# Optimization experiments

Measured on AMD Instinct MI355X. Metric: run time of the kernel, lower is better.

## Reference

```python
import jax, jax.numpy as jnp
import numpy as np

EMBED_DIM = 1024
NUM_HEADS = 16
HEAD_DIM = EMBED_DIM // NUM_HEADS


def setup_inputs() -> dict:
    key = jax.random.key(0)
    ks = jax.random.split(key, 9)
    D = EMBED_DIM
    s = 1.0 / np.sqrt(D)
    x = jax.random.normal(ks[0], (2, 2048, D), dtype=jnp.float32)
    Wq = jax.random.uniform(ks[1], (D, D), jnp.float32, -s, s)
    bq = jax.random.uniform(ks[2], (D,), jnp.float32, -s, s)
    Wk = jax.random.uniform(ks[3], (D, D), jnp.float32, -s, s)
    bk = jax.random.uniform(ks[4], (D,), jnp.float32, -s, s)
    Wv = jax.random.uniform(ks[5], (D, D), jnp.float32, -s, s)
    bv = jax.random.uniform(ks[6], (D,), jnp.float32, -s, s)
    Wo = jax.random.uniform(ks[7], (D, D), jnp.float32, -s, s)
    bo = jax.random.uniform(ks[8], (D,), jnp.float32, -s, s)
    return {"x": x, "Wq": Wq, "bq": bq, "Wk": Wk, "bk": bk,
            "Wv": Wv, "bv": bv, "Wo": Wo, "bo": bo}


def reference(x, Wq, bq, Wk, bk, Wv, bv, Wo, bo):
    B, N, D = x.shape
    H, Dh = NUM_HEADS, HEAD_DIM
    # QKV projections (weights stored as [in, out] = torch W.T)
    q = (x @ Wq + bq).reshape(B, N, H, Dh).transpose(0, 2, 1, 3)  # b h n d
    k = (x @ Wk + bk).reshape(B, N, H, Dh).transpose(0, 2, 1, 3)
    v = (x @ Wv + bv).reshape(B, N, H, Dh).transpose(0, 2, 1, 3)
    # NOTE: original divides by head_dim (not sqrt(head_dim))
    scores = jnp.einsum('bhnd,bhmd->bhnm', q, k) / Dh
    probs = jax.nn.softmax(scores, axis=-1)
    out = jnp.einsum('bhnm,bhmd->bhnd', probs, v)  # b h n d
    out = out.transpose(0, 2, 1, 3).reshape(B, N, D)
    return out @ Wo + bo
```

## Files before the change

### kernel.cpp

```cpp
#include <hip/hip_runtime.h>
#include <hip/hip_bf16.h>

constexpr int EMBED = 1024;
constexpr int NHEAD = 16;
constexpr int HDIM  = 64;
constexpr int BATCH = 2;
constexpr int SEQ   = 2048;
constexpr int MROWS = BATCH * SEQ;
constexpr int NKB   = EMBED / 32;
constexpr int NT    = SEQ / 64;

typedef __attribute__((ext_vector_type(8)))  short          bf8;
typedef __attribute__((ext_vector_type(8)))  unsigned short us8;
typedef __attribute__((ext_vector_type(16))) float          f32x16;
typedef __attribute__((ext_vector_type(2)))  int            i32x2;

__device__ __forceinline__ unsigned short f2bf(float f) {
  unsigned u = __float_as_uint(f);
  u += 0x7fffu + ((u >> 16) & 1u);
  return (unsigned short)(u >> 16);
}
__device__ __forceinline__ float bf2f(unsigned short h) {
  return __uint_as_float((unsigned)h << 16);
}
__device__ __forceinline__ void async16(const void* g, void* l) {
  __builtin_amdgcn_global_load_lds(
      (const __attribute__((address_space(1))) unsigned int*)g,
      (__attribute__((address_space(3))) unsigned int*)l, 16, 0, 0);
}
__device__ __forceinline__ i32x2 swap32(int a, int b) {
  return __builtin_amdgcn_permlane32_swap(a, b, false, false);
}
__device__ __forceinline__ unsigned cvt2(float a, float b) {
  union { __hip_bfloat162 bb; unsigned u; } cv;
  cv.bb = __float22bfloat162_rn(float2{a, b});
  return cv.u;
}
__device__ __forceinline__ void bar_pre() {
  __builtin_amdgcn_s_barrier();
  __builtin_amdgcn_sched_barrier(0);
}
__device__ __forceinline__ void bar_post() {
  __builtin_amdgcn_sched_barrier(0);
  __builtin_amdgcn_s_barrier();
}

__global__ __launch_bounds__(256) void pack_x_k(
    const float* __restrict__ x, char* __restrict__ Xp)
{
  int sid = blockIdx.x * 256 + threadIdx.x;
  int s = sid & 7, t = (sid >> 3) & 31, u = sid >> 8;
  int c = s ^ (u & 7);
  int par = c >> 2, kq = c & 3;
  const float* src = x + (size_t)(2 * u + par) * EMBED + t * 32 + kq * 8;
  us8 o;
  #pragma unroll
  for (int e = 0; e < 8; ++e) o[e] = f2bf(src[e]);
  *(us8*)(Xp + ((size_t)sid << 4)) = o;
}

__global__ __launch_bounds__(256) void pack_w_lds_k(
    const float* __restrict__ W0, const float* __restrict__ W1,
    const float* __restrict__ W2, const float* __restrict__ W3,
    char* __restrict__ Wpk)
{
  __shared__ float LDSf[8 * 1032];
  const int blk = blockIdx.x;
  const int tid = threadIdx.x;
  const int y = blk >> 7, r = blk & 127, t = r >> 2, q = r & 3;
  const float* W = (y == 0) ? W0 : (y == 1) ? W1 : (y == 2) ? W2 : W3;
  char* op = Wpk + ((size_t)y << 21);

  #pragma unroll
  for (int it = 0; it < 8; ++it) {
    int f4 = it * 256 + tid;
    int row = f4 >> 8, col4 = (f4 & 255) << 2;
    float4 v = *(const float4*)(W + (size_t)(t * 32 + q * 8 + row) * EMBED + col4);
    *(float4*)(&LDSf[row * 1032 + col4]) = v;
  }
  __syncthreads();

  #pragma unroll
  for (int it = 0; it < 4; ++it) {
    int sid2 = it * 256 + tid;
    int u = sid2 >> 1, par = sid2 & 1;
    int s = ((par << 2) | q) ^ (u & 7);
    us8 o;
    #pragma unroll
    for (int e = 0; e < 8; ++e) o[e] = f2bf(LDSf[e * 1032 + 2 * u + par]);
    *(us8*)(op + (((size_t)(u << 8) + (t << 3) + s) << 4)) = o;
  }
}

__global__ __launch_bounds__(256) void gemm_qkv_fused_k(
    const char* __restrict__ Apk, const char* __restrict__ Wpk,
    const float* __restrict__ B0, const float* __restrict__ B1, const float* __restrict__ B2,
    unsigned short* __restrict__ Qbf, unsigned short* __restrict__ Kbf,
    unsigned short* __restrict__ Vt)
{
  __shared__ __align__(16) char lds[65536];

  const int tid  = threadIdx.x;
  const int lane = tid & 63;
  const int wid  = tid >> 6;
  const int wr   = wid >> 1, wc = wid & 1;
  const int ln31 = lane & 31, lhalf = lane >> 5;

  const int bid = blockIdx.x;
  const int swz = (bid & 7) * 32 + (bid >> 3);
  const int rp  = swz >> 3, cb = swz & 7;

  const int M0 = rp * 128, N0 = cb * 128;
  const int U0 = M0 >> 1, V0 = N0 >> 1;

  const char* ab[2]; const char* wbase[2]; int ldoff[2];
  #pragma unroll
  for (int i = 0; i < 2; ++i) {
    int idx = i * 256 + tid;
    int ul = idx >> 3, sl = idx & 7;
    ab[i]    = Apk + ((size_t)(U0 + ul) << 12) + (sl << 4);
    wbase[i] = Wpk + ((size_t)(V0 + ul) << 12) + (sl << 4);
    ldoff[i] = i * 4096 + (tid >> 6) * 1024;
  }

  f32x16 acc[3][2][2];
  #pragma unroll
  for (int z = 0; z < 3; ++z)
    #pragma unroll
    for (int mi = 0; mi < 2; ++mi)
      #pragma unroll
      for (int ni = 0; ni < 2; ++ni)
        #pragma unroll
        for (int q = 0; q < 16; ++q) acc[z][mi][ni][q] = 0.f;

  #pragma unroll
  for (int i = 0; i < 2; ++i) {
    async16(ab[i], lds + ldoff[i]);
    #pragma unroll
    for (int z = 0; z < 3; ++z)
      async16(wbase[i] + ((size_t)z << 21), lds + 8192 + z * 8192 + ldoff[i]);
  }

  for (int t = 0; t < NKB; ++t) {
    const int c = t & 1;
    if (t + 1 < NKB) {
      const int off = (t + 1) << 7;
      #pragma unroll
      for (int i = 0; i < 2; ++i) {
        async16(ab[i] + off, lds + (c ^ 1) * 32768 + ldoff[i]);
        #pragma unroll
        for (int z = 0; z < 3; ++z)
          async16(wbase[i] + ((size_t)z << 21) + off,
                  lds + (c ^ 1) * 32768 + 8192 + z * 8192 + ldoff[i]);
      }
      asm volatile("s_waitcnt vmcnt(8)" ::: "memory");
    } else {
      asm volatile("s_waitcnt vmcnt(0)" ::: "memory");
    }
    bar_pre();
    const char* Ab = lds + c * 32768;
    const char* Wb = Ab + 8192;
    #pragma unroll
    for (int kb = 0; kb < 2; ++kb) {
      const int kq = (kb << 1) | lhalf;
      bf8 a[2];
      #pragma unroll
      for (int mi = 0; mi < 2; ++mi) {
        int m = wr * 64 + mi * 32 + ln31;
        int u = m >> 1;
        int s = (((m & 1) << 2) | kq) ^ (u & 7);
        a[mi] = *(const bf8*)(Ab + u * 128 + s * 16);
      }
      #pragma unroll
      for (int z = 0; z < 3; ++z) {
        bf8 b[2];
        #pragma unroll
        for (int ni = 0; ni < 2; ++ni) {
          int n = wc * 64 + ni * 32 + ln31;
          int u = n >> 1;
          int s = (((n & 1) << 2) | kq) ^ (u & 7);
          b[ni] = *(const bf8*)(Wb + z * 8192 + u * 128 + s * 16);
        }
        #pragma unroll
        for (int mi = 0; mi < 2; ++mi)
          #pragma unroll
          for (int ni = 0; ni < 2; ++ni)
            acc[z][mi][ni] = __builtin_amdgcn_mfma_f32_32x32x16_bf16(
                a[mi], b[ni], acc[z][mi][ni], 0, 0, 0);
      }
    }
    bar_post();
  }

  #pragma unroll
  for (int z = 0; z < 2; ++z) {
    unsigned short* Cb = (z == 0) ? Qbf : Kbf;
    const float* Bv = (z == 0) ? B0 : B1;
    const float sc = (z == 0) ? (1.44269504088896f / 64.0f) : 1.0f;
    #pragma unroll
    for (int ni = 0; ni < 2; ++ni) {
      int col = N0 + wc * 64 + ni * 32 + ln31;
      float bb = Bv[col];
      #pragma unroll
      for (int mi = 0; mi < 2; ++mi)
        #pragma unroll
        for (int r = 0; r < 16; ++r) {
          int row = M0 + wr * 64 + mi * 32 + (r & 3) + ((r >> 2) << 3) + (lhalf << 2);
          Cb[(size_t)row * EMBED + col] = f2bf((acc[z][mi][ni][r] + bb) * sc);
        }
    }
  }
  {
    const int tg0 = (M0 & 2047) >> 6;
    const int bb  = M0 >> 11;
    #pragma unroll
    for (int ni = 0; ni < 2; ++ni) {
      int col = N0 + wc * 64 + ni * 32 + ln31;
      int hh = col >> 6, dl = col & 63;
      float bv = B2[col];
      size_t base2 = (((size_t)(bb * 16 + hh)) << 17) + ((size_t)(tg0 + wr) << 12) + (dl << 6);
      unsigned pkq[2][4][2];
      #pragma unroll
      for (int mi = 0; mi < 2; ++mi)
        #pragma unroll
        for (int rg = 0; rg < 4; ++rg) {
          pkq[mi][rg][0] = cvt2(acc[2][mi][ni][4 * rg + 0] + bv, acc[2][mi][ni][4 * rg + 1] + bv);
          pkq[mi][rg][1] = cvt2(acc[2][mi][ni][4 * rg + 2] + bv, acc[2][mi][ni][4 * rg + 3] + bv);
        }
      #pragma unroll
      for (int gk = 0; gk < 8; ++gk) {
        const int mi = gk >> 2, rg = gk & 3;
        i32x2 e0 = swap32((int)pkq[mi][rg][0], (int)pkq[mi][rg][0]);
        i32x2 e1 = swap32((int)pkq[mi][rg][1], (int)pkq[mi][rg][1]);
        int g = gk ^ (dl & 7);
        if ((g >> 2) == lhalf) {
          union { unsigned u[4]; us8 v; } o;
          o.u[0] = (unsigned)e0[0]; o.u[1] = (unsigned)e1[0];
          o.u[2] = (unsigned)e0[1]; o.u[3] = (unsigned)e1[1];
          *(us8*)(Vt + base2 + (g << 3)) = o.v;
        }
      }
    }
  }
}

__global__ __launch_bounds__(256) void gemm_out_bf16_k(
    const char* __restrict__ Apk, const char* __restrict__ Wpk,
    const float* __restrict__ Bv, float* __restrict__ Cf)
{
  __shared__ __align__(16) char lds[65536];

  const int tid  = threadIdx.x;
  const int lane = tid & 63;
  const int wid  = tid >> 6;
  const int wr   = wid >> 1, wc = wid & 1;
  const int ln31 = lane & 31, lhalf = lane >> 5;

  const int bid = blockIdx.x;
  const int swz = (bid & 7) * 32 + (bid >> 3);
  const int rp  = swz >> 3, cb = swz & 7;

  const int M0 = rp * 128, N0 = cb * 128;
  const int U0 = M0 >> 1, V0 = N0 >> 1;

  const char* ab[4]; const char* wb[4]; int ldoff[4];
  #pragma unroll
  for (int i = 0; i < 4; ++i) {
    int idx = i * 256 + tid;
    int ul = idx >> 4, tt = (idx >> 3) & 1, sl = idx & 7;
    ab[i] = Apk + ((size_t)(U0 + ul) << 12) + (tt << 7) + (sl << 4);
    wb[i] = Wpk + ((size_t)(V0 + ul) << 12) + (tt << 7) + (sl << 4);
    ldoff[i] = i * 4096 + (tid >> 6) * 1024;
  }

  f32x16 acc[2][2];
  #pragma unroll
  for (int mi = 0; mi < 2; ++mi)
    #pragma unroll
    for (int ni = 0; ni < 2; ++ni)
      #pragma unroll
      for (int q = 0; q < 16; ++q) acc[mi][ni][q] = 0.f;

  #pragma unroll
  for (int i = 0; i < 4; ++i) {
    async16(ab[i], lds + ldoff[i]);
    async16(wb[i], lds + 16384 + ldoff[i]);
  }

  for (int T = 0; T < NKB / 2; ++T) {
    const int c = T & 1;
    if (T + 1 < NKB / 2) {
      const int off = (T + 1) << 8;
      #pragma unroll
      for (int i = 0; i < 4; ++i) {
        async16(ab[i] + off, lds + (c ^ 1) * 32768 + ldoff[i]);
        async16(wb[i] + off, lds + (c ^ 1) * 32768 + 16384 + ldoff[i]);
      }
      asm volatile("s_waitcnt vmcnt(8)" ::: "memory");
    } else {
      asm volatile("s_waitcnt vmcnt(0)" ::: "memory");
    }
    bar_pre();
    const char* Ab = lds + c * 32768;
    const char* Wb = Ab + 16384;
    #pragma unroll
    for (int tt = 0; tt < 2; ++tt) {
      #pragma unroll
      for (int kb = 0; kb < 2; ++kb) {
        const int kq = (kb << 1) | lhalf;
        bf8 a[2], b[2];
        #pragma unroll
        for (int mi = 0; mi < 2; ++mi) {
          int m = wr * 64 + mi * 32 + ln31;
          int ul = m >> 1;
          int s = (((m & 1) << 2) | kq) ^ (ul & 7);
          a[mi] = *(const bf8*)(Ab + ul * 256 + tt * 128 + s * 16);
        }
        #pragma unroll
        for (int ni = 0; ni < 2; ++ni) {
          int n = wc * 64 + ni * 32 + ln31;
          int ul = n >> 1;
          int s = (((n & 1) << 2) | kq) ^ (ul & 7);
          b[ni] = *(const bf8*)(Wb + ul * 256 + tt * 128 + s * 16);
        }
        #pragma unroll
        for (int mi = 0; mi < 2; ++mi)
          #pragma unroll
          for (int ni = 0; ni < 2; ++ni)
            acc[mi][ni] = __builtin_amdgcn_mfma_f32_32x32x16_bf16(
                a[mi], b[ni], acc[mi][ni], 0, 0, 0);
      }
    }
    bar_post();
  }

  #pragma unroll
  for (int ni = 0; ni < 2; ++ni) {
    int col = N0 + wc * 64 + ni * 32 + ln31;
    float bb = Bv[col];
    #pragma unroll
    for (int mi = 0; mi < 2; ++mi)
      #pragma unroll
      for (int r = 0; r < 16; ++r) {
        int row = M0 + wr * 64 + mi * 32 + (r & 3) + ((r >> 2) << 3) + (lhalf << 2);
        Cf[(size_t)row * EMBED + col] = acc[mi][ni][r] + bb;
      }
  }
}

__global__ __launch_bounds__(512) void attn_mfma_k(
    const unsigned short* __restrict__ Qb, const unsigned short* __restrict__ Kb,
    const char* __restrict__ Vt, char* __restrict__ A2)
{
  __shared__ __align__(16) char lds[65536];

  const int bid = blockIdx.x;
  const int swz = (bid & 7) * 64 + (bid >> 3);
  const int qt = swz & 15, h = (swz >> 4) & 15, b = swz >> 8;

  const int tid  = threadIdx.x;
  const int kw   = tid >> 8;
  const int tidg = tid & 255;
  const int lane = tid & 63;
  const int qw   = (tid >> 6) & 3;
  const int ln31 = lane & 31, lh = lane >> 5;
  const int l7   = ln31 & 7;

  const int q0 = qt * 128;
  const int sbase = kw * 32768;
  const int T0 = kw * 16;

  bf8 qf[4];
  {
    const size_t qoff = (size_t)(b * SEQ + q0 + qw * 32 + ln31) * EMBED + h * HDIM;
    #pragma unroll
    for (int kd = 0; kd < 4; ++kd)
      qf[kd] = *(const bf8*)(Qb + qoff + (2 * kd + lh) * 8);
  }

  const unsigned short* ksrc[2];
  const char* vtb = Vt + ((size_t)(b * 16 + h) << 18);
  int ldoff[2];
  #pragma unroll
  for (int i = 0; i < 2; ++i) {
    int idx = i * 256 + tidg;
    int r = idx >> 3, s7 = idx & 7;
    int un = s7 ^ (r & 7);
    ksrc[i] = Kb + (size_t)(b * SEQ + r) * EMBED + h * HDIM + un * 8;
    ldoff[i] = i * 4096 + (tidg >> 6) * 1024;
  }

  #pragma unroll
  for (int i = 0; i < 2; ++i) {
    async16(ksrc[i] + (size_t)(T0 * 64) * EMBED, lds + sbase + ldoff[i]);
    async16(vtb + (T0 << 13) + ((i * 256 + tidg) << 4), lds + sbase + 8192 + ldoff[i]);
  }

  const bf8 ones = {0x3F80, 0x3F80, 0x3F80, 0x3F80, 0x3F80, 0x3F80, 0x3F80, 0x3F80};
  f32x16 z16;
  #pragma unroll
  for (int r = 0; r < 16; ++r) z16[r] = 0.f;

  f32x16 oacc[2], oacc3;
  #pragma unroll
  for (int df = 0; df < 2; ++df)
    #pragma unroll
    for (int r = 0; r < 16; ++r) oacc[df][r] = 0.f;
  oacc3 = z16;

  for (int it = 0; it < NT / 2; ++it) {
    const int c = it & 1;
    if (it + 1 < NT / 2) {
      const int tn = T0 + it + 1;
      #pragma unroll
      for (int i = 0; i < 2; ++i) {
        async16(ksrc[i] + (size_t)(tn * 64) * EMBED, lds + sbase + (c ^ 1) * 16384 + ldoff[i]);
        async16(vtb + (tn << 13) + ((i * 256 + tidg) << 4),
                lds + sbase + (c ^ 1) * 16384 + 8192 + ldoff[i]);
      }
      asm volatile("s_waitcnt vmcnt(4)" ::: "memory");
    } else {
      asm volatile("s_waitcnt vmcnt(0)" ::: "memory");
    }
    bar_pre();
    const char* Kbuf = lds + sbase + c * 16384;
    const char* Vbuf = Kbuf + 8192;

    f32x16 sacc[2];
    __builtin_amdgcn_s_setprio(1);
    #pragma unroll
    for (int kf = 0; kf < 2; ++kf) {
      bf8 ka0 = *(const bf8*)(Kbuf + (32 * kf + ln31) * 128 + ((lh ^ l7) << 4));
      sacc[kf] = __builtin_amdgcn_mfma_f32_32x32x16_bf16(ka0, qf[0], z16, 0, 0, 0);
      #pragma unroll
      for (int kd = 1; kd < 4; ++kd) {
        bf8 ka = *(const bf8*)(Kbuf + (32 * kf + ln31) * 128 + (((2 * kd + lh) ^ l7) << 4));
        sacc[kf] = __builtin_amdgcn_mfma_f32_32x32x16_bf16(ka, qf[kd], sacc[kf], 0, 0, 0);
      }
    }
    __builtin_amdgcn_s_setprio(0);

    unsigned pk[2][8];
    #pragma unroll
    for (int g = 0; g < 4; ++g)
      #pragma unroll
      for (int j = 0; j < 2; ++j)
        pk[0][2 * g + j] = cvt2(__builtin_amdgcn_exp2f(sacc[0][4 * g + 2 * j]),
                                __builtin_amdgcn_exp2f(sacc[0][4 * g + 2 * j + 1]));
    __builtin_amdgcn_s_setprio(1);
    #pragma unroll
    for (int kb = 0; kb < 2; ++kb) {
      const int b4 = (kb & 1) * 4;
      i32x2 r02 = swap32((int)pk[0][b4 + 0], (int)pk[0][b4 + 2]);
      i32x2 r13 = swap32((int)pk[0][b4 + 1], (int)pk[0][b4 + 3]);
      union { unsigned u[4]; bf8 v; } pf;
      pf.u[0] = (unsigned)r02[0]; pf.u[1] = (unsigned)r13[0];
      pf.u[2] = (unsigned)r02[1]; pf.u[3] = (unsigned)r13[1];
      #pragma unroll
      for (int df = 0; df < 2; ++df) {
        bf8 va = *(const bf8*)(Vbuf + (32 * df + ln31) * 128 + (((2 * kb + lh) ^ l7) << 4));
        oacc[df] = __builtin_amdgcn_mfma_f32_32x32x16_bf16(va, pf.v, oacc[df], 0, 0, 0);
      }
      oacc3 = __builtin_amdgcn_mfma_f32_32x32x16_bf16(ones, pf.v, oacc3, 0, 0, 0);
    }
    __builtin_amdgcn_s_setprio(0);
    #pragma unroll
    for (int g = 0; g < 4; ++g)
      #pragma unroll
      for (int j = 0; j < 2; ++j)
        pk[1][2 * g + j] = cvt2(__builtin_amdgcn_exp2f(sacc[1][4 * g + 2 * j]),
                                __builtin_amdgcn_exp2f(sacc[1][4 * g + 2 * j + 1]));
    __builtin_amdgcn_s_setprio(1);
    #pragma unroll
    for (int kb = 2; kb < 4; ++kb) {
      const int b4 = (kb & 1) * 4;
      i32x2 r02 = swap32((int)pk[1][b4 + 0], (int)pk[1][b4 + 2]);
      i32x2 r13 = swap32((int)pk[1][b4 + 1], (int)pk[1][b4 + 3]);
      union { unsigned u[4]; bf8 v; } pf;
      pf.u[0] = (unsigned)r02[0]; pf.u[1] = (unsigned)r13[0];
      pf.u[2] = (unsigned)r02[1]; pf.u[3] = (unsigned)r13[1];
      #pragma unroll
      for (int df = 0; df < 2; ++df) {
        bf8 va = *(const bf8*)(Vbuf + (32 * df + ln31) * 128 + (((2 * kb + lh) ^ l7) << 4));
        oacc[df] = __builtin_amdgcn_mfma_f32_32x32x16_bf16(va, pf.v, oacc[df], 0, 0, 0);
      }
      oacc3 = __builtin_amdgcn_mfma_f32_32x32x16_bf16(ones, pf.v, oacc3, 0, 0, 0);
    }
    __builtin_amdgcn_s_setprio(0);
    bar_post();
  }

  float* ex = (float*)lds;
  const int slot = qw * 64 + lane;
  if (kw == 1) {
    #pragma unroll
    for (int df = 0; df < 2; ++df)
      #pragma unroll
      for (int r = 0; r < 16; ++r)
        ex[slot * 34 + df * 16 + r] = oacc[df][r];
    ex[slot * 34 + 32] = oacc3[0];
  }
  __syncthreads();
  if (kw == 1) return;

  #pragma unroll
  for (int df = 0; df < 2; ++df)
    #pragma unroll
    for (int r = 0; r < 16; ++r)
      oacc[df][r] += ex[slot * 34 + df * 16 + r];
  const float ltot = oacc3[0] + ex[slot * 34 + 32];

  const float inv = 1.0f / ltot;
  float fl[8][4], fh[8][4];
  #pragma unroll
  for (int df = 0; df < 2; ++df)
    #pragma unroll
    for (int r = 0; r < 16; ++r) {
      float o = oacc[df][r] * inv;
      i32x2 rr = swap32(__float_as_int(o), __float_as_int(o));
      fl[df * 4 + (r >> 2)][r & 3] = __int_as_float(rr[0]);
      fh[df * 4 + (r >> 2)][r & 3] = __int_as_float(rr[1]);
    }

  const int row = b * SEQ + q0 + qw * 32 + ln31;
  const int u = row >> 1, par = row & 1;
  #pragma unroll
  for (int g = 0; g < 8; ++g) {
    us8 hi;
    #pragma unroll
    for (int e = 0; e < 8; ++e) {
      float f = (e < 4) ? fl[g][e] : fh[g][e - 4];
      hi[e] = f2bf(f);
    }
    int t_blk = 2 * h + (g >> 2), kq = g & 3;
    size_t ub = ((size_t)(u * 32 + t_blk)) << 7;
    int s = ((par << 2) | kq) ^ (u & 7);
    *(us8*)(A2 + ub + (s << 4)) = hi;
  }
}

extern "C" void kernel_launch(void* const* d_in, const int* in_sizes, int n_in,
                              void* d_out, int out_size, void* d_ws, size_t ws_size,
                              hipStream_t stream)
{
  const float* x  = (const float*)d_in[0];
  const float* Wq = (const float*)d_in[1];
  const float* bq = (const float*)d_in[2];
  const float* Wk = (const float*)d_in[3];
  const float* bk = (const float*)d_in[4];
  const float* Wv = (const float*)d_in[5];
  const float* bv = (const float*)d_in[6];
  const float* Wo = (const float*)d_in[7];
  const float* bo = (const float*)d_in[8];
  float* out = (float*)d_out;

  char* wsb = (char*)d_ws;
  char*           Xp  = wsb;
  char*           Wpk = wsb + ((size_t)8  << 20);
  unsigned short* Qbf = (unsigned short*)(wsb + ((size_t)16 << 20));
  unsigned short* Kbf = (unsigned short*)(wsb + ((size_t)24 << 20));
  unsigned short* Vtp = (unsigned short*)(wsb + ((size_t)32 << 20));
  char*           A2  = wsb + ((size_t)40 << 20);

  pack_x_k<<<dim3(2048), dim3(256), 0, stream>>>(x, Xp);
  pack_w_lds_k<<<dim3(512), dim3(256), 0, stream>>>(Wq, Wk, Wv, Wo, Wpk);

  gemm_qkv_fused_k<<<dim3(256), dim3(256), 0, stream>>>(
      Xp, Wpk, bq, bk, bv, Qbf, Kbf, Vtp);

  attn_mfma_k<<<dim3(512), dim3(512), 0, stream>>>(
      Qbf, Kbf, (const char*)Vtp, A2);

  gemm_out_bf16_k<<<dim3(256), dim3(256), 0, stream>>>(
      A2, Wpk + ((size_t)3 << 21), bo, out);
}
```

Before: 112.0 us.

## Halve GEMM M-tile to 64 rows, double grids, merge pack kernels

Both projection GEMMs now use 64x128 output tiles with each of the four waves owning a 32-column strip, which doubles the grid from 256 to 512 blocks so more of the GPU's compute units get work. LDS per block shrinks to match. The x and weight packing kernels are merged into a single launch to remove one kernel launch gap. In exchange, the weight tiles are reloaded twice as often, so arithmetic intensity per block drops.

```diff
diff --git a/kernel.cpp b/kernel.cpp
--- a/kernel.cpp
+++ b/kernel.cpp
@@ -20,9 +20,6 @@
   u += 0x7fffu + ((u >> 16) & 1u);
   return (unsigned short)(u >> 16);
 }
-__device__ __forceinline__ float bf2f(unsigned short h) {
-  return __uint_as_float((unsigned)h << 16);
-}
 __device__ __forceinline__ void async16(const void* g, void* l) {
   __builtin_amdgcn_global_load_lds(
       (const __attribute__((address_space(1))) unsigned int*)g,
@@ -45,50 +42,48 @@
   __builtin_amdgcn_s_barrier();
 }
 
-__global__ __launch_bounds__(256) void pack_x_k(
-    const float* __restrict__ x, char* __restrict__ Xp)
-{
-  int sid = blockIdx.x * 256 + threadIdx.x;
-  int s = sid & 7, t = (sid >> 3) & 31, u = sid >> 8;
-  int c = s ^ (u & 7);
-  int par = c >> 2, kq = c & 3;
-  const float* src = x + (size_t)(2 * u + par) * EMBED + t * 32 + kq * 8;
-  us8 o;
-  #pragma unroll
-  for (int e = 0; e < 8; ++e) o[e] = f2bf(src[e]);
-  *(us8*)(Xp + ((size_t)sid << 4)) = o;
-}
-
-__global__ __launch_bounds__(256) void pack_w_lds_k(
+__global__ __launch_bounds__(256) void pack_all2_k(
+    const float* __restrict__ x,
     const float* __restrict__ W0, const float* __restrict__ W1,
     const float* __restrict__ W2, const float* __restrict__ W3,
-    char* __restrict__ Wpk)
+    char* __restrict__ Xp, char* __restrict__ Wpk)
 {
   __shared__ float LDSf[8 * 1032];
   const int blk = blockIdx.x;
   const int tid = threadIdx.x;
-  const int y = blk >> 7, r = blk & 127, t = r >> 2, q = r & 3;
-  const float* W = (y == 0) ? W0 : (y == 1) ? W1 : (y == 2) ? W2 : W3;
-  char* op = Wpk + ((size_t)y << 21);
-
-  #pragma unroll
-  for (int it = 0; it < 8; ++it) {
-    int f4 = it * 256 + tid;
-    int row = f4 >> 8, col4 = (f4 & 255) << 2;
-    float4 v = *(const float4*)(W + (size_t)(t * 32 + q * 8 + row) * EMBED + col4);
-    *(float4*)(&LDSf[row * 1032 + col4]) = v;
-  }
-  __syncthreads();
-
-  #pragma unroll
-  for (int it = 0; it < 4; ++it) {
-    int sid2 = it * 256 + tid;
-    int u = sid2 >> 1, par = sid2 & 1;
-    int s = ((par << 2) | q) ^ (u & 7);
+  if (blk < 2048) {
+    int sid = blk * 256 + tid;
+    int s = sid & 7, t = (sid >> 3) & 31, u = sid >> 8;
+    int c = s ^ (u & 7);
+    int par = c >> 2, kq = c & 3;
+    const float* src = x + (size_t)(2 * u + par) * EMBED + t * 32 + kq * 8;
     us8 o;
     #pragma unroll
-    for (int e = 0; e < 8; ++e) o[e] = f2bf(LDSf[e * 1032 + 2 * u + par]);
-    *(us8*)(op + (((size_t)(u << 8) + (t << 3) + s) << 4)) = o;
+    for (int e = 0; e < 8; ++e) o[e] = f2bf(src[e]);
+    *(us8*)(Xp + ((size_t)sid << 4)) = o;
+  } else {
+    const int bb = blk - 2048;
+    const int y = bb >> 7, r = bb & 127, t = r >> 2, q = r & 3;
+    const float* W = (y == 0) ? W0 : (y == 1) ? W1 : (y == 2) ? W2 : W3;
+    char* op = Wpk + ((size_t)y << 21);
+    #pragma unroll
+    for (int it = 0; it < 8; ++it) {
+      int f4 = it * 256 + tid;
+      int row = f4 >> 8, col4 = (f4 & 255) << 2;
+      float4 v = *(const float4*)(W + (size_t)(t * 32 + q * 8 + row) * EMBED + col4);
+      *(float4*)(&LDSf[row * 1032 + col4]) = v;
+    }
+    __syncthreads();
+    #pragma unroll
+    for (int it = 0; it < 4; ++it) {
+      int sid2 = it * 256 + tid;
+      int u = sid2 >> 1, par = sid2 & 1;
+      int s = ((par << 2) | q) ^ (u & 7);
+      us8 o;
+      #pragma unroll
+      for (int e = 0; e < 8; ++e) o[e] = f2bf(LDSf[e * 1032 + 2 * u + par]);
+      *(us8*)(op + (((size_t)(u << 8) + (t << 3) + s) << 4)) = o;
+    }
   }
 }
 
@@ -98,147 +93,127 @@
     unsigned short* __restrict__ Qbf, unsigned short* __restrict__ Kbf,
     unsigned short* __restrict__ Vt)
 {
-  __shared__ __align__(16) char lds[65536];
+  __shared__ __align__(16) char lds[57344];
 
   const int tid  = threadIdx.x;
   const int lane = tid & 63;
   const int wid  = tid >> 6;
-  const int wr   = wid >> 1, wc = wid & 1;
   const int ln31 = lane & 31, lhalf = lane >> 5;
 
   const int bid = blockIdx.x;
-  const int swz = (bid & 7) * 32 + (bid >> 3);
+  const int swz = (bid & 7) * 64 + (bid >> 3);
   const int rp  = swz >> 3, cb = swz & 7;
 
-  const int M0 = rp * 128, N0 = cb * 128;
-  const int U0 = M0 >> 1, V0 = N0 >> 1;
-
-  const char* ab[2]; const char* wbase[2]; int ldoff[2];
+  const int M0 = rp * 64, N0 = cb * 128;
+  const int U0 = rp * 32, V0 = cb * 64;
+
+  const char* ab = Apk + ((size_t)(U0 + (tid >> 3)) << 12) + ((tid & 7) << 4);
+  const int la = tid * 16;
+  const char* wb[2]; int lw[2];
   #pragma unroll
   for (int i = 0; i < 2; ++i) {
     int idx = i * 256 + tid;
-    int ul = idx >> 3, sl = idx & 7;
-    ab[i]    = Apk + ((size_t)(U0 + ul) << 12) + (sl << 4);
-    wbase[i] = Wpk + ((size_t)(V0 + ul) << 12) + (sl << 4);
-    ldoff[i] = i * 4096 + (tid >> 6) * 1024;
-  }
-
-  f32x16 acc[3][2][2];
+    wb[i] = Wpk + ((size_t)(V0 + (idx >> 3)) << 12) + ((idx & 7) << 4);
+    lw[i] = 4096 + i * 4096 + tid * 16;
+  }
+
+  f32x16 acc[3][2];
   #pragma unroll
   for (int z = 0; z < 3; ++z)
     #pragma unroll
     for (int mi = 0; mi < 2; ++mi)
       #pragma unroll
-      for (int ni = 0; ni < 2; ++ni)
-        #pragma unroll
-        for (int q = 0; q < 16; ++q) acc[z][mi][ni][q] = 0.f;
-
-  #pragma unroll
-  for (int i = 0; i < 2; ++i) {
-    async16(ab[i], lds + ldoff[i]);
-    #pragma unroll
-    for (int z = 0; z < 3; ++z)
-      async16(wbase[i] + ((size_t)z << 21), lds + 8192 + z * 8192 + ldoff[i]);
-  }
+      for (int q = 0; q < 16; ++q) acc[z][mi][q] = 0.f;
+
+  async16(ab, lds + la);
+  #pragma unroll
+  for (int z = 0; z < 3; ++z)
+    #pragma unroll
+    for (int i = 0; i < 2; ++i)
+      async16(wb[i] + ((size_t)z << 21), lds + z * 8192 + lw[i]);
 
   for (int t = 0; t < NKB; ++t) {
     const int c = t & 1;
     if (t + 1 < NKB) {
       const int off = (t + 1) << 7;
-      #pragma unroll
-      for (int i = 0; i < 2; ++i) {
-        async16(ab[i] + off, lds + (c ^ 1) * 32768 + ldoff[i]);
+      async16(ab + off, lds + (c ^ 1) * 28672 + la);
+      #pragma unroll
+      for (int z = 0; z < 3; ++z)
         #pragma unroll
-        for (int z = 0; z < 3; ++z)
-          async16(wbase[i] + ((size_t)z << 21) + off,
-                  lds + (c ^ 1) * 32768 + 8192 + z * 8192 + ldoff[i]);
-      }
-      asm volatile("s_waitcnt vmcnt(8)" ::: "memory");
+        for (int i = 0; i < 2; ++i)
+          async16(wb[i] + ((size_t)z << 21) + off,
+                  lds + (c ^ 1) * 28672 + z * 8192 + lw[i]);
+      asm volatile("s_waitcnt vmcnt(7)" ::: "memory");
     } else {
       asm volatile("s_waitcnt vmcnt(0)" ::: "memory");
     }
     bar_pre();
-    const char* Ab = lds + c * 32768;
-    const char* Wb = Ab + 8192;
+    const char* Ab = lds + c * 28672;
+    const char* Wb = Ab + 4096;
     #pragma unroll
     for (int kb = 0; kb < 2; ++kb) {
       const int kq = (kb << 1) | lhalf;
       bf8 a[2];
       #pragma unroll
       for (int mi = 0; mi < 2; ++mi) {
-        int m = wr * 64 + mi * 32 + ln31;
+        int m = mi * 32 + ln31;
         int u = m >> 1;
         int s = (((m & 1) << 2) | kq) ^ (u & 7);
         a[mi] = *(const bf8*)(Ab + u * 128 + s * 16);
       }
+      const int n = wid * 32 + ln31;
+      const int un = n >> 1;
+      const int sn = (((n & 1) << 2) | kq) ^ (un & 7);
       #pragma unroll
       for (int z = 0; z < 3; ++z) {
-        bf8 b[2];
-        #pragma unroll
-        for (int ni = 0; ni < 2; ++ni) {
-          int n = wc * 64 + ni * 32 + ln31;
-          int u = n >> 1;
-          int s = (((n & 1) << 2) | kq) ^ (u & 7);
-          b[ni] = *(const bf8*)(Wb + z * 8192 + u * 128 + s * 16);
-        }
-        #pragma unroll
-        for (int mi = 0; mi < 2; ++mi)
-          #pragma unroll
-          for (int ni = 0; ni < 2; ++ni)
-            acc[z][mi][ni] = __builtin_amdgcn_mfma_f32_32x32x16_bf16(
-                a[mi], b[ni], acc[z][mi][ni], 0, 0, 0);
+        bf8 b = *(const bf8*)(Wb + z * 8192 + un * 128 + sn * 16);
+        acc[z][0] = __builtin_amdgcn_mfma_f32_32x32x16_bf16(a[0], b, acc[z][0], 0, 0, 0);
+        acc[z][1] = __builtin_amdgcn_mfma_f32_32x32x16_bf16(a[1], b, acc[z][1], 0, 0, 0);
       }
     }
     bar_post();
   }
 
+  const int col = N0 + wid * 32 + ln31;
   #pragma unroll
   for (int z = 0; z < 2; ++z) {
     unsigned short* Cb = (z == 0) ? Qbf : Kbf;
     const float* Bv = (z == 0) ? B0 : B1;
     const float sc = (z == 0) ? (1.44269504088896f / 64.0f) : 1.0f;
-    #pragma unroll
-    for (int ni = 0; ni < 2; ++ni) {
-      int col = N0 + wc * 64 + ni * 32 + ln31;
-      float bb = Bv[col];
-      #pragma unroll
-      for (int mi = 0; mi < 2; ++mi)
-        #pragma unroll
-        for (int r = 0; r < 16; ++r) {
-          int row = M0 + wr * 64 + mi * 32 + (r & 3) + ((r >> 2) << 3) + (lhalf << 2);
-          Cb[(size_t)row * EMBED + col] = f2bf((acc[z][mi][ni][r] + bb) * sc);
-        }
-    }
+    float bb = Bv[col];
+    #pragma unroll
+    for (int mi = 0; mi < 2; ++mi)
+      #pragma unroll
+      for (int r = 0; r < 16; ++r) {
+        int row = M0 + mi * 32 + (r & 3) + ((r >> 2) << 3) + (lhalf << 2);
+        Cb[(size_t)row * EMBED + col] = f2bf((acc[z][mi][r] + bb) * sc);
+      }
   }
   {
-    const int tg0 = (M0 & 2047) >> 6;
-    const int bb  = M0 >> 11;
-    #pragma unroll
-    for (int ni = 0; ni < 2; ++ni) {
-      int col = N0 + wc * 64 + ni * 32 + ln31;
-      int hh = col >> 6, dl = col & 63;
-      float bv = B2[col];
-      size_t base2 = (((size_t)(bb * 16 + hh)) << 17) + ((size_t)(tg0 + wr) << 12) + (dl << 6);
-      unsigned pkq[2][4][2];
-      #pragma unroll
-      for (int mi = 0; mi < 2; ++mi)
-        #pragma unroll
-        for (int rg = 0; rg < 4; ++rg) {
-          pkq[mi][rg][0] = cvt2(acc[2][mi][ni][4 * rg + 0] + bv, acc[2][mi][ni][4 * rg + 1] + bv);
-          pkq[mi][rg][1] = cvt2(acc[2][mi][ni][4 * rg + 2] + bv, acc[2][mi][ni][4 * rg + 3] + bv);
-        }
-      #pragma unroll
-      for (int gk = 0; gk < 8; ++gk) {
-        const int mi = gk >> 2, rg = gk & 3;
-        i32x2 e0 = swap32((int)pkq[mi][rg][0], (int)pkq[mi][rg][0]);
-        i32x2 e1 = swap32((int)pkq[mi][rg][1], (int)pkq[mi][rg][1]);
-        int g = gk ^ (dl & 7);
-        if ((g >> 2) == lhalf) {
-          union { unsigned u[4]; us8 v; } o;
-          o.u[0] = (unsigned)e0[0]; o.u[1] = (unsigned)e1[0];
-          o.u[2] = (unsigned)e0[1]; o.u[3] = (unsigned)e1[1];
-          *(us8*)(Vt + base2 + (g << 3)) = o.v;
-        }
+    const int tile = (M0 & 2047) >> 6;
+    const int bb   = M0 >> 11;
+    const int hh = col >> 6, dl = col & 63;
+    const float bv = B2[col];
+    size_t base2 = (((size_t)(bb * 16 + hh)) << 17) + ((size_t)tile << 12) + (dl << 6);
+    unsigned pkq[2][4][2];
+    #pragma unroll
+    for (int mi = 0; mi < 2; ++mi)
+      #pragma unroll
+      for (int rg = 0; rg < 4; ++rg) {
+        pkq[mi][rg][0] = cvt2(acc[2][mi][4 * rg + 0] + bv, acc[2][mi][4 * rg + 1] + bv);
+        pkq[mi][rg][1] = cvt2(acc[2][mi][4 * rg + 2] + bv, acc[2][mi][4 * rg + 3] + bv);
+      }
+    #pragma unroll
+    for (int gk = 0; gk < 8; ++gk) {
+      const int mi = gk >> 2, rg = gk & 3;
+      i32x2 e0 = swap32((int)pkq[mi][rg][0], (int)pkq[mi][rg][0]);
+      i32x2 e1 = swap32((int)pkq[mi][rg][1], (int)pkq[mi][rg][1]);
+      int g = gk ^ (dl & 7);
+      if ((g >> 2) == lhalf) {
+        union { unsigned u[4]; us8 v; } o;
+        o.u[0] = (unsigned)e0[0]; o.u[1] = (unsigned)e1[0];
+        o.u[2] = (unsigned)e0[1]; o.u[3] = (unsigned)e1[1];
+        *(us8*)(Vt + base2 + (g << 3)) = o.v;
       }
     }
   }
@@ -248,104 +223,96 @@
     const char* __restrict__ Apk, const char* __restrict__ Wpk,
     const float* __restrict__ Bv, float* __restrict__ Cf)
 {
-  __shared__ __align__(16) char lds[65536];
+  __shared__ __align__(16) char lds[49152];
 
   const int tid  = threadIdx.x;
   const int lane = tid & 63;
   const int wid  = tid >> 6;
-  const int wr   = wid >> 1, wc = wid & 1;
   const int ln31 = lane & 31, lhalf = lane >> 5;
 
   const int bid = blockIdx.x;
-  const int swz = (bid & 7) * 32 + (bid >> 3);
+  const int swz = (bid & 7) * 64 + (bid >> 3);
   const int rp  = swz >> 3, cb = swz & 7;
 
-  const int M0 = rp * 128, N0 = cb * 128;
-  const int U0 = M0 >> 1, V0 = N0 >> 1;
-
-  const char* ab[4]; const char* wb[4]; int ldoff[4];
-  #pragma unroll
-  for (int i = 0; i < 4; ++i) {
+  const int M0 = rp * 64, N0 = cb * 128;
+  const int U0 = rp * 32, V0 = cb * 64;
+
+  const char* ab[2]; int la[2];
+  #pragma unroll
+  for (int i = 0; i < 2; ++i) {
     int idx = i * 256 + tid;
     int ul = idx >> 4, tt = (idx >> 3) & 1, sl = idx & 7;
     ab[i] = Apk + ((size_t)(U0 + ul) << 12) + (tt << 7) + (sl << 4);
-    wb[i] = Wpk + ((size_t)(V0 + ul) << 12) + (tt << 7) + (sl << 4);
-    ldoff[i] = i * 4096 + (tid >> 6) * 1024;
-  }
-
-  f32x16 acc[2][2];
+    la[i] = i * 4096 + tid * 16;
+  }
+  const char* wb[4]; int lw[4];
+  #pragma unroll
+  for (int j = 0; j < 4; ++j) {
+    int idx = j * 256 + tid;
+    int ul = idx >> 4, tt = (idx >> 3) & 1, sl = idx & 7;
+    wb[j] = Wpk + ((size_t)(V0 + ul) << 12) + (tt << 7) + (sl << 4);
+    lw[j] = 8192 + j * 4096 + tid * 16;
+  }
+
+  f32x16 acc[2];
   #pragma unroll
   for (int mi = 0; mi < 2; ++mi)
     #pragma unroll
-    for (int ni = 0; ni < 2; ++ni)
-      #pragma unroll
-      for (int q = 0; q < 16; ++q) acc[mi][ni][q] = 0.f;
-
-  #pragma unroll
-  for (int i = 0; i < 4; ++i) {
-    async16(ab[i], lds + ldoff[i]);
-    async16(wb[i], lds + 16384 + ldoff[i]);
-  }
+    for (int q = 0; q < 16; ++q) acc[mi][q] = 0.f;
+
+  #pragma unroll
+  for (int i = 0; i < 2; ++i) async16(ab[i], lds + la[i]);
+  #pragma unroll
+  for (int j = 0; j < 4; ++j) async16(wb[j], lds + lw[j]);
 
   for (int T = 0; T < NKB / 2; ++T) {
     const int c = T & 1;
     if (T + 1 < NKB / 2) {
       const int off = (T + 1) << 8;
       #pragma unroll
-      for (int i = 0; i < 4; ++i) {
-        async16(ab[i] + off, lds + (c ^ 1) * 32768 + ldoff[i]);
-        async16(wb[i] + off, lds + (c ^ 1) * 32768 + 16384 + ldoff[i]);
-      }
-      asm volatile("s_waitcnt vmcnt(8)" ::: "memory");
+      for (int i = 0; i < 2; ++i) async16(ab[i] + off, lds + (c ^ 1) * 24576 + la[i]);
+      #pragma unroll
+      for (int j = 0; j < 4; ++j) async16(wb[j] + off, lds + (c ^ 1) * 24576 + lw[j]);
+      asm volatile("s_waitcnt vmcnt(6)" ::: "memory");
     } else {
       asm volatile("s_waitcnt vmcnt(0)" ::: "memory");
     }
     bar_pre();
-    const char* Ab = lds + c * 32768;
-    const char* Wb = Ab + 16384;
+    const char* Ab = lds + c * 24576;
+    const char* Wb = Ab + 8192;
     #pragma unroll
     for (int tt = 0; tt < 2; ++tt) {
       #pragma unroll
       for (int kb = 0; kb < 2; ++kb) {
         const int kq = (kb << 1) | lhalf;
-        bf8 a[2], b[2];
+        bf8 a[2];
         #pragma unroll
         for (int mi = 0; mi < 2; ++mi) {
-          int m = wr * 64 + mi * 32 + ln31;
-          int ul = m >> 1;
-          int s = (((m & 1) << 2) | kq) ^ (ul & 7);
-          a[mi] = *(const bf8*)(Ab + ul * 256 + tt * 128 + s * 16);
+          int m = mi * 32 + ln31;
+          int u = m >> 1;
+          int s = (((m & 1) << 2) | kq) ^ (u & 7);
+          a[mi] = *(const bf8*)(Ab + u * 256 + tt * 128 + s * 16);
         }
-        #pragma unroll
-        for (int ni = 0; ni < 2; ++ni) {
-          int n = wc * 64 + ni * 32 + ln31;
-          int ul = n >> 1;
-          int s = (((n & 1) << 2) | kq) ^ (ul & 7);
-          b[ni] = *(const bf8*)(Wb + ul * 256 + tt * 128 + s * 16);
-        }
-        #pragma unroll
-        for (int mi = 0; mi < 2; ++mi)
-          #pragma unroll
-          for (int ni = 0; ni < 2; ++ni)
-            acc[mi][ni] = __builtin_amdgcn_mfma_f32_32x32x16_bf16(
-                a[mi], b[ni], acc[mi][ni], 0, 0, 0);
+        const int n = wid * 32 + ln31;
+        const int un = n >> 1;
+        const int sn = (((n & 1) << 2) | kq) ^ (un & 7);
+        bf8 b = *(const bf8*)(Wb + un * 256 + tt * 128 + sn * 16);
+        acc[0] = __builtin_amdgcn_mfma_f32_32x32x16_bf16(a[0], b, acc[0], 0, 0, 0);
+        acc[1] = __builtin_amdgcn_mfma_f32_32x32x16_bf16(a[1], b, acc[1], 0, 0, 0);
       }
     }
     bar_post();
   }
 
-  #pragma unroll
-  for (int ni = 0; ni < 2; ++ni) {
-    int col = N0 + wc * 64 + ni * 32 + ln31;
-    float bb = Bv[col];
-    #pragma unroll
-    for (int mi = 0; mi < 2; ++mi)
-      #pragma unroll
-      for (int r = 0; r < 16; ++r) {
-        int row = M0 + wr * 64 + mi * 32 + (r & 3) + ((r >> 2) << 3) + (lhalf << 2);
-        Cf[(size_t)row * EMBED + col] = acc[mi][ni][r] + bb;
-      }
-  }
+  const int col = N0 + wid * 32 + ln31;
+  const float bb = Bv[col];
+  #pragma unroll
+  for (int mi = 0; mi < 2; ++mi)
+    #pragma unroll
+    for (int r = 0; r < 16; ++r) {
+      int row = M0 + mi * 32 + (r & 3) + ((r >> 2) << 3) + (lhalf << 2);
+      Cf[(size_t)row * EMBED + col] = acc[mi][r] + bb;
+    }
 }
 
 __global__ __launch_bounds__(512) void attn_mfma_k(
@@ -562,15 +529,15 @@
   unsigned short* Vtp = (unsigned short*)(wsb + ((size_t)32 << 20));
   char*           A2  = wsb + ((size_t)40 << 20);
 
-  pack_x_k<<<dim3(2048), dim3(256), 0, stream>>>(x, Xp);
-  pack_w_lds_k<<<dim3(512), dim3(256), 0, stream>>>(Wq, Wk, Wv, Wo, Wpk);
-
-  gemm_qkv_fused_k<<<dim3(256), dim3(256), 0, stream>>>(
+  pack_all2_k<<<dim3(2560), dim3(256), 0, stream>>>(
+      x, Wq, Wk, Wv, Wo, Xp, Wpk);
+
+  gemm_qkv_fused_k<<<dim3(512), dim3(256), 0, stream>>>(
       Xp, Wpk, bq, bk, bv, Qbf, Kbf, Vtp);
 
   attn_mfma_k<<<dim3(512), dim3(512), 0, stream>>>(
       Qbf, Kbf, (const char*)Vtp, A2);
 
-  gemm_out_bf16_k<<<dim3(256), dim3(256), 0, stream>>>(
+  gemm_out_bf16_k<<<dim3(512), dim3(256), 0, stream>>>(
       A2, Wpk + ((size_t)3 << 21), bo, out);
 }
```

Measured after the change: 110.3 us, median of 2. Within noise of the previous version (-1.6%).
